# Performance work log

Hardware: AMD Instinct MI355X
Metric: run time of the kernel (lower is better)

The kernel has to match this reference:

```python
import jax, jax.numpy as jnp
import numpy as np


def setup_inputs() -> dict:
    key = jax.random.key(0)
    k1, k2 = jax.random.split(key)
    seqs = jax.random.normal(k1, (16, 2048, 256), dtype=jnp.float32)
    durations = jax.random.randint(k2, (16, 2048), 0, 4, dtype=jnp.int32)
    return {"seqs": seqs, "durations": durations}


def reference(seqs, durations):
    # seqs: [N, T, M] float; durations: [N, T] int
    N, T, M = seqs.shape
    lens = durations.sum(axis=1)                      # [N] upsampled lengths
    max_len = int(jnp.max(lens))                      # padded output length
    pos = jnp.arange(max_len)                         # [L]
    cum = jnp.cumsum(durations, axis=1)               # [N, T] exclusive bounds
    # source token index for each output slot: number of cum entries <= pos
    idx = jax.vmap(lambda c: jnp.searchsorted(c, pos, side='right'))(cum)  # [N, L]
    idx = jnp.clip(idx, 0, T - 1)
    gathered = jnp.take_along_axis(seqs, idx[:, :, None], axis=1)          # [N, L, M]
    mask = pos[None, :] < lens[:, None]               # valid (non-padded) slots
    upsampled = jnp.where(mask[:, :, None], gathered, jnp.zeros((), seqs.dtype))
    return upsampled, lens
```

## Files before the change

### kernel.cpp

```cpp
#include <hip/hip_runtime.h>


#define N_ROWS 16
#define T_LEN  2048
#define M_DIM  256
#define M_VEC  (M_DIM / 4)
#define W_TOK  4

typedef float f32x4 __attribute__((ext_vector_type(4)));

__global__ __launch_bounds__(256) void cumsum_kernel(
    const int* __restrict__ dur, int* __restrict__ cum,
    float* __restrict__ lens_out) {
  const int n = blockIdx.x;
  const int tid = threadIdx.x;
  const int lane = tid & 63;
  const int wv = tid >> 6;
  const int base = n * T_LEN + tid * 8;

  int4 a = *(const int4*)(dur + base);
  int4 b = *(const int4*)(dur + base + 4);

  int tot = 0;
  a.x = (tot += a.x); a.y = (tot += a.y); a.z = (tot += a.z); a.w = (tot += a.w);
  b.x = (tot += b.x); b.y = (tot += b.y); b.z = (tot += b.z); b.w = (tot += b.w);

  int scan = tot;
#pragma unroll
  for (int d = 1; d < 64; d <<= 1) {
    int t = __shfl_up(scan, d, 64);
    if (lane >= d) scan += t;
  }

  __shared__ int wtot[4];
  if (lane == 63) wtot[wv] = scan;
  __syncthreads();

  int woff = 0;
#pragma unroll
  for (int w = 0; w < 3; ++w) woff += (w < wv) ? wtot[w] : 0;

  const int excl = woff + scan - tot;
  a.x += excl; a.y += excl; a.z += excl; a.w += excl;
  b.x += excl; b.y += excl; b.z += excl; b.w += excl;
  *(int4*)(cum + base) = a;
  *(int4*)(cum + base + 4) = b;

  if (tid == 255) lens_out[n] = (float)(woff + scan);
}

__global__ __launch_bounds__(256) void scatter_kernel(
    const f32x4* __restrict__ seqs4, const int* __restrict__ cum,
    f32x4* __restrict__ out4, int max_len) {
  const int lane = threadIdx.x & 63;
  const int wave = threadIdx.x >> 6;
  const int n = blockIdx.y;
  const int p = (blockIdx.x * 4 + wave) * W_TOK;

  const int* __restrict__ c = cum + n * T_LEN;
  const int len = c[T_LEN - 1];

  int cb = 0;
  if (lane <= W_TOK) {
    int j = p - 1 + lane;
    if (j < 0) j = 0; else if (j >= T_LEN) j = T_LEN - 1;
    cb = (p - 1 + lane < 0) ? 0 : c[j];
  }

  int st[W_TOK], dk[W_TOK];
#pragma unroll
  for (int k = 0; k < W_TOK; ++k) {
    const int c0 = __shfl(cb, k, 64);
    const int c1 = __shfl(cb, k + 1, 64);
    st[k] = c0;
    dk[k] = (p + k < T_LEN) ? (c1 - c0) : 0;
  }

  const f32x4* __restrict__ srow = seqs4 + (size_t)n * T_LEN * M_VEC + lane;
  f32x4* __restrict__ orow = out4 + (size_t)n * max_len * M_VEC + lane;

  f32x4 v[W_TOK];
#pragma unroll
  for (int k = 0; k < W_TOK; ++k) {
    v[k] = (f32x4)0.f;
    if (dk[k] > 0) v[k] = srow[(size_t)(p + k) * M_VEC];
  }

#pragma unroll
  for (int k = 0; k < W_TOK; ++k) {
    if (dk[k] > 0) orow[(size_t)(st[k] + 0) * M_VEC] = v[k];
    if (dk[k] > 1) orow[(size_t)(st[k] + 1) * M_VEC] = v[k];
    if (dk[k] > 2) orow[(size_t)(st[k] + 2) * M_VEC] = v[k];
  }

  const f32x4 z = (f32x4)0.f;
#pragma unroll
  for (int k = 0; k < W_TOK; ++k) {
    const int i = p + k;
    if (i >= len && i < max_len) orow[(size_t)i * M_VEC] = z;
  }
}

extern "C" void kernel_launch(void* const* d_in, const int* in_sizes, int n_in,
                              void* d_out, int out_size, void* d_ws, size_t ws_size,
                              hipStream_t stream) {
  const float* seqs = (const float*)d_in[0];
  const int* durations = (const int*)d_in[1];
  float* out = (float*)d_out;

  const int N = N_ROWS;
  const int M = M_DIM;
  const int max_len = (out_size - N) / (N * M);

  int* cum = (int*)d_ws;
  float* lens_out = out + (size_t)N * max_len * M;

  cumsum_kernel<<<dim3(N), dim3(256), 0, stream>>>(durations, cum, lens_out);

  const int span = (max_len > T_LEN) ? max_len : T_LEN;
  dim3 grid((span + 4 * W_TOK - 1) / (4 * W_TOK), N);
  scatter_kernel<<<grid, dim3(256), 0, stream>>>(
      (const f32x4*)seqs, cum, (f32x4*)out, max_len);
}
```

Measured before the change: 22.47 us.

## Replace full cumsum with per-group offsets and in-wave local scan

The first kernel now writes only 64 group prefix offsets per row (one per 32 tokens) plus the row lengths, rather than a full 2048-entry cumulative sum. The scatter kernel rebuilds token start positions from the durations with a 32-lane shuffle scan added to the group offset. Source rows are now loaded unconditionally, even for zero-duration tokens. This is meant to cut the prologue kernel's work and the workspace traffic between the kernels, at the cost of extra shuffles and redundant source loads in the scatter kernel.

```diff
diff --git a/kernel.cpp b/kernel.cpp
--- a/kernel.cpp
+++ b/kernel.cpp
@@ -6,75 +6,47 @@
 #define M_DIM  256
 #define M_VEC  (M_DIM / 4)
 #define W_TOK  4
+#define GRP    32
 
 typedef float f32x4 __attribute__((ext_vector_type(4)));
 
-__global__ __launch_bounds__(256) void cumsum_kernel(
-    const int* __restrict__ dur, int* __restrict__ cum,
-    float* __restrict__ lens_out) {
+__global__ __launch_bounds__(64) void pregroup_kernel(
+    const int* __restrict__ dur, int* __restrict__ gp,
+    int* __restrict__ lens_i, float* __restrict__ lens_out) {
   const int n = blockIdx.x;
-  const int tid = threadIdx.x;
-  const int lane = tid & 63;
-  const int wv = tid >> 6;
-  const int base = n * T_LEN + tid * 8;
-
-  int4 a = *(const int4*)(dur + base);
-  int4 b = *(const int4*)(dur + base + 4);
+  const int lane = threadIdx.x;
+  const int base = n * T_LEN + lane * GRP;
 
   int tot = 0;
-  a.x = (tot += a.x); a.y = (tot += a.y); a.z = (tot += a.z); a.w = (tot += a.w);
-  b.x = (tot += b.x); b.y = (tot += b.y); b.z = (tot += b.z); b.w = (tot += b.w);
+#pragma unroll
+  for (int j = 0; j < GRP / 4; ++j) {
+    const int4 v = *(const int4*)(dur + base + j * 4);
+    tot += v.x + v.y + v.z + v.w;
+  }
 
   int scan = tot;
 #pragma unroll
   for (int d = 1; d < 64; d <<= 1) {
-    int t = __shfl_up(scan, d, 64);
+    const int t = __shfl_up(scan, d, 64);
     if (lane >= d) scan += t;
   }
 
-  __shared__ int wtot[4];
-  if (lane == 63) wtot[wv] = scan;
-  __syncthreads();
-
-  int woff = 0;
-#pragma unroll
-  for (int w = 0; w < 3; ++w) woff += (w < wv) ? wtot[w] : 0;
-
-  const int excl = woff + scan - tot;
-  a.x += excl; a.y += excl; a.z += excl; a.w += excl;
-  b.x += excl; b.y += excl; b.z += excl; b.w += excl;
-  *(int4*)(cum + base) = a;
-  *(int4*)(cum + base + 4) = b;
-
-  if (tid == 255) lens_out[n] = (float)(woff + scan);
+  gp[(n << 6) + lane] = scan - tot;
+  if (lane == 63) {
+    lens_i[n] = scan;
+    lens_out[n] = (float)scan;
+  }
 }
 
 __global__ __launch_bounds__(256) void scatter_kernel(
-    const f32x4* __restrict__ seqs4, const int* __restrict__ cum,
+    const f32x4* __restrict__ seqs4, const int* __restrict__ dur,
+    const int* __restrict__ gp, const int* __restrict__ lens_i,
     f32x4* __restrict__ out4, int max_len) {
   const int lane = threadIdx.x & 63;
   const int wave = threadIdx.x >> 6;
   const int n = blockIdx.y;
   const int p = (blockIdx.x * 4 + wave) * W_TOK;
-
-  const int* __restrict__ c = cum + n * T_LEN;
-  const int len = c[T_LEN - 1];
-
-  int cb = 0;
-  if (lane <= W_TOK) {
-    int j = p - 1 + lane;
-    if (j < 0) j = 0; else if (j >= T_LEN) j = T_LEN - 1;
-    cb = (p - 1 + lane < 0) ? 0 : c[j];
-  }
-
-  int st[W_TOK], dk[W_TOK];
-#pragma unroll
-  for (int k = 0; k < W_TOK; ++k) {
-    const int c0 = __shfl(cb, k, 64);
-    const int c1 = __shfl(cb, k + 1, 64);
-    st[k] = c0;
-    dk[k] = (p + k < T_LEN) ? (c1 - c0) : 0;
-  }
+  const bool tok = (p < T_LEN);
 
   const f32x4* __restrict__ srow = seqs4 + (size_t)n * T_LEN * M_VEC + lane;
   f32x4* __restrict__ orow = out4 + (size_t)n * max_len * M_VEC + lane;
@@ -83,14 +55,38 @@
 #pragma unroll
   for (int k = 0; k < W_TOK; ++k) {
     v[k] = (f32x4)0.f;
-    if (dk[k] > 0) v[k] = srow[(size_t)(p + k) * M_VEC];
+    if (tok) v[k] = srow[(size_t)(p + k) * M_VEC];
   }
 
+  const int len = lens_i[n];
+
+  if (tok) {
+    const int g = p >> 5;
+    const int q = p & 31;
+    int dl = (lane < GRP) ? dur[n * T_LEN + (g << 5) + lane] : 0;
+    int sc = dl;
 #pragma unroll
-  for (int k = 0; k < W_TOK; ++k) {
-    if (dk[k] > 0) orow[(size_t)(st[k] + 0) * M_VEC] = v[k];
-    if (dk[k] > 1) orow[(size_t)(st[k] + 1) * M_VEC] = v[k];
-    if (dk[k] > 2) orow[(size_t)(st[k] + 2) * M_VEC] = v[k];
+    for (int d = 1; d < GRP; d <<= 1) {
+      const int t = __shfl_up(sc, d, 64);
+      if (lane >= d) sc += t;
+    }
+    const int base_gp = gp[(n << 6) + g];
+
+    int st[W_TOK], dk[W_TOK];
+#pragma unroll
+    for (int k = 0; k < W_TOK; ++k) {
+      const int j = q + k;
+      const int incl_prev = (j == 0) ? 0 : __shfl(sc, j - 1, 64);
+      st[k] = base_gp + incl_prev;
+      dk[k] = __shfl(dl, j, 64);
+    }
+
+#pragma unroll
+    for (int k = 0; k < W_TOK; ++k) {
+      if (dk[k] > 0) orow[(size_t)(st[k] + 0) * M_VEC] = v[k];
+      if (dk[k] > 1) orow[(size_t)(st[k] + 1) * M_VEC] = v[k];
+      if (dk[k] > 2) orow[(size_t)(st[k] + 2) * M_VEC] = v[k];
+    }
   }
 
   const f32x4 z = (f32x4)0.f;
@@ -112,13 +108,15 @@
   const int M = M_DIM;
   const int max_len = (out_size - N) / (N * M);
 
-  int* cum = (int*)d_ws;
+  int* gp = (int*)d_ws;
+  int* lens_i = gp + N_ROWS * 64;
   float* lens_out = out + (size_t)N * max_len * M;
 
-  cumsum_kernel<<<dim3(N), dim3(256), 0, stream>>>(durations, cum, lens_out);
+  pregroup_kernel<<<dim3(N), dim3(64), 0, stream>>>(
+      durations, gp, lens_i, lens_out);
 
   const int span = (max_len > T_LEN) ? max_len : T_LEN;
   dim3 grid((span + 4 * W_TOK - 1) / (4 * W_TOK), N);
   scatter_kernel<<<grid, dim3(256), 0, stream>>>(
-      (const f32x4*)seqs, cum, (f32x4*)out, max_len);
+      (const f32x4*)seqs, durations, gp, lens_i, (f32x4*)out, max_len);
 }
```

New measurement: 23.78 us. +5.8%, slower.

## Fuse cumsum into scatter kernel with per-block redundant scan in LDS

Applied to the files above, without the earlier changes.

Drops the separate cumsum kernel. Every scatter block now recomputes the full per-row prefix sum of durations into shared memory, so the inter-kernel dependency, the launch and the global workspace round-trip are gone. Seq loads are issued before the scan so their latency can overlap with it. The cost is redundant work: each of the many blocks per row reads the whole 8KB duration row and runs a block scan with two barriers. The blocks also load seqs unconditionally, even for zero-duration tokens.

```diff
diff --git a/kernel.cpp b/kernel.cpp
--- a/kernel.cpp
+++ b/kernel.cpp
@@ -6,75 +6,19 @@
 #define M_DIM  256
 #define M_VEC  (M_DIM / 4)
 #define W_TOK  4
+#define BLK_POS 16
 
 typedef float f32x4 __attribute__((ext_vector_type(4)));
 
-__global__ __launch_bounds__(256) void cumsum_kernel(
-    const int* __restrict__ dur, int* __restrict__ cum,
-    float* __restrict__ lens_out) {
-  const int n = blockIdx.x;
+__global__ __launch_bounds__(256) void fused_upsample_kernel(
+    const f32x4* __restrict__ seqs4, const int* __restrict__ dur,
+    f32x4* __restrict__ out4, float* __restrict__ lens_out, int max_len) {
   const int tid = threadIdx.x;
   const int lane = tid & 63;
-  const int wv = tid >> 6;
-  const int base = n * T_LEN + tid * 8;
-
-  int4 a = *(const int4*)(dur + base);
-  int4 b = *(const int4*)(dur + base + 4);
-
-  int tot = 0;
-  a.x = (tot += a.x); a.y = (tot += a.y); a.z = (tot += a.z); a.w = (tot += a.w);
-  b.x = (tot += b.x); b.y = (tot += b.y); b.z = (tot += b.z); b.w = (tot += b.w);
-
-  int scan = tot;
-#pragma unroll
-  for (int d = 1; d < 64; d <<= 1) {
-    int t = __shfl_up(scan, d, 64);
-    if (lane >= d) scan += t;
-  }
-
-  __shared__ int wtot[4];
-  if (lane == 63) wtot[wv] = scan;
-  __syncthreads();
-
-  int woff = 0;
-#pragma unroll
-  for (int w = 0; w < 3; ++w) woff += (w < wv) ? wtot[w] : 0;
-
-  const int excl = woff + scan - tot;
-  a.x += excl; a.y += excl; a.z += excl; a.w += excl;
-  b.x += excl; b.y += excl; b.z += excl; b.w += excl;
-  *(int4*)(cum + base) = a;
-  *(int4*)(cum + base + 4) = b;
-
-  if (tid == 255) lens_out[n] = (float)(woff + scan);
-}
-
-__global__ __launch_bounds__(256) void scatter_kernel(
-    const f32x4* __restrict__ seqs4, const int* __restrict__ cum,
-    f32x4* __restrict__ out4, int max_len) {
-  const int lane = threadIdx.x & 63;
-  const int wave = threadIdx.x >> 6;
+  const int wave = tid >> 6;
   const int n = blockIdx.y;
-  const int p = (blockIdx.x * 4 + wave) * W_TOK;
-
-  const int* __restrict__ c = cum + n * T_LEN;
-  const int len = c[T_LEN - 1];
-
-  int cb = 0;
-  if (lane <= W_TOK) {
-    int j = p - 1 + lane;
-    if (j < 0) j = 0; else if (j >= T_LEN) j = T_LEN - 1;
-    cb = (p - 1 + lane < 0) ? 0 : c[j];
-  }
-
-  int st[W_TOK], dk[W_TOK];
-#pragma unroll
-  for (int k = 0; k < W_TOK; ++k) {
-    const int c0 = __shfl(cb, k, 64);
-    const int c1 = __shfl(cb, k + 1, 64);
-    st[k] = c0;
-    dk[k] = (p + k < T_LEN) ? (c1 - c0) : 0;
-  }
+  const int p = blockIdx.x * BLK_POS + wave * W_TOK;
+  const bool tok = (p < T_LEN);
 
   const f32x4* __restrict__ srow = seqs4 + (size_t)n * T_LEN * M_VEC + lane;
   f32x4* __restrict__ orow = out4 + (size_t)n * max_len * M_VEC + lane;
@@ -83,14 +27,56 @@
 #pragma unroll
   for (int k = 0; k < W_TOK; ++k) {
     v[k] = (f32x4)0.f;
-    if (dk[k] > 0) v[k] = srow[(size_t)(p + k) * M_VEC];
+    if (tok) v[k] = srow[(size_t)(p + k) * M_VEC];
   }
 
+  __shared__ int cums[T_LEN];
+  __shared__ int wtot[4];
+  const int base = n * T_LEN + tid * 8;
+  int4 a = *(const int4*)(dur + base);
+  int4 b = *(const int4*)(dur + base + 4);
+  int tot = 0;
+  a.x = (tot += a.x); a.y = (tot += a.y); a.z = (tot += a.z); a.w = (tot += a.w);
+  b.x = (tot += b.x); b.y = (tot += b.y); b.z = (tot += b.z); b.w = (tot += b.w);
+
+  int scan = tot;
 #pragma unroll
-  for (int k = 0; k < W_TOK; ++k) {
-    if (dk[k] > 0) orow[(size_t)(st[k] + 0) * M_VEC] = v[k];
-    if (dk[k] > 1) orow[(size_t)(st[k] + 1) * M_VEC] = v[k];
-    if (dk[k] > 2) orow[(size_t)(st[k] + 2) * M_VEC] = v[k];
+  for (int d = 1; d < 64; d <<= 1) {
+    const int t = __shfl_up(scan, d, 64);
+    if (lane >= d) scan += t;
+  }
+  if (lane == 63) wtot[wave] = scan;
+  __syncthreads();
+  int woff = 0;
+#pragma unroll
+  for (int w = 0; w < 3; ++w) woff += (w < wave) ? wtot[w] : 0;
+
+  const int excl = woff + scan - tot;
+  a.x += excl; a.y += excl; a.z += excl; a.w += excl;
+  b.x += excl; b.y += excl; b.z += excl; b.w += excl;
+  *(int4*)(cums + tid * 8) = a;
+  *(int4*)(cums + tid * 8 + 4) = b;
+  __syncthreads();
+
+  const int len = cums[T_LEN - 1];
+
+  if (blockIdx.x == 0 && tid == 0) lens_out[n] = (float)len;
+
+  if (tok) {
+    int st[W_TOK], dk[W_TOK];
+#pragma unroll
+    for (int k = 0; k < W_TOK; ++k) {
+      const int c0 = (p + k == 0) ? 0 : cums[p + k - 1];
+      const int c1 = cums[p + k];
+      st[k] = c0;
+      dk[k] = c1 - c0;
+    }
+#pragma unroll
+    for (int k = 0; k < W_TOK; ++k) {
+      if (dk[k] > 0) orow[(size_t)(st[k] + 0) * M_VEC] = v[k];
+      if (dk[k] > 1) orow[(size_t)(st[k] + 1) * M_VEC] = v[k];
+      if (dk[k] > 2) orow[(size_t)(st[k] + 2) * M_VEC] = v[k];
+    }
   }
 
   const f32x4 z = (f32x4)0.f;
@@ -112,13 +98,10 @@
   const int M = M_DIM;
   const int max_len = (out_size - N) / (N * M);
 
-  int* cum = (int*)d_ws;
   float* lens_out = out + (size_t)N * max_len * M;
 
-  cumsum_kernel<<<dim3(N), dim3(256), 0, stream>>>(durations, cum, lens_out);
-
   const int span = (max_len > T_LEN) ? max_len : T_LEN;
-  dim3 grid((span + 4 * W_TOK - 1) / (4 * W_TOK), N);
-  scatter_kernel<<<grid, dim3(256), 0, stream>>>(
-      (const f32x4*)seqs, cum, (f32x4*)out, max_len);
+  dim3 grid((span + BLK_POS - 1) / BLK_POS, N);
+  fused_upsample_kernel<<<grid, dim3(256), 0, stream>>>(
+      (const f32x4*)seqs, durations, (f32x4*)out, lens_out, max_len);
 }
```

New measurement: 19.54 us. -13.0%, faster.
